# Optimization experiments

Hardware: AMD Instinct MI355X
Metric: run time of the kernel (lower is better)

Reference implementation:

```python
import jax, jax.numpy as jnp
import numpy as np

N = 1_000_000          # number of fusion candidate pairs
H, W = 200, 70400      # sparse buffer dims hard-coded in the module
FILL = -9999999.0


def _init_conv(k, co, ci):
    # torch Conv2d default init: U(-1/sqrt(fan_in), 1/sqrt(fan_in)), 1x1 kernel
    bound = 1.0 / np.sqrt(ci)
    kw, kb = jax.random.split(k)
    w = jax.random.uniform(kw, (co, ci), jnp.float32, -bound, bound)
    b = jax.random.uniform(kb, (co,), jnp.float32, -bound, bound)
    return w, b


def setup_inputs() -> dict:
    key = jax.random.key(0)
    ks = jax.random.split(key, 7)
    input_1 = jax.random.normal(ks[0], (1, 4, 1, N), dtype=jnp.float32)
    idx0 = jax.random.randint(ks[1], (N,), 0, H)   # row in [0,200)
    idx1 = jax.random.randint(ks[2], (N,), 0, W)   # col in [0,70400)
    tensor_index = jnp.stack([idx0, idx1], axis=1).astype(jnp.int64)
    w1, b1 = _init_conv(ks[3], 18, 4)
    w2, b2 = _init_conv(ks[4], 36, 18)
    w3, b3 = _init_conv(ks[5], 36, 36)
    w4, b4 = _init_conv(ks[6], 1, 36)
    return dict(input_1=input_1, tensor_index=tensor_index,
                w1=w1, b1=b1, w2=w2, b2=b2, w3=w3, b3=b3, w4=w4, b4=b4)


def _fuse_2d_3d(x, w1, b1, w2, b2, w3, b3, w4, b4):
    # x: (4, N); 1x1 convs over a (1,C,1,N) tensor == per-point channel matmuls
    h = jax.nn.relu(w1 @ x + b1[:, None])
    h = jax.nn.relu(w2 @ h + b2[:, None])
    h = jax.nn.relu(w3 @ h + b3[:, None])
    return w4 @ h + b4[:, None]  # (1, N)


def reference(input_1, tensor_index, w1, b1, w2, b2, w3, b3, w4, b4):
    base = jnp.full((1, H, W), FILL, dtype=input_1.dtype)

    def scatter_branch(_):
        feat = _fuse_2d_3d(input_1[0, :, 0, :], w1, b1, w2, b2, w3, b3, w4, b4)  # (1, N)
        out = base.at[:, tensor_index[:, 0], tensor_index[:, 1]].set(feat)
        return out, jnp.int32(1)

    def empty_branch(_):
        return base, jnp.int32(0)

    out_1, flag = jax.lax.cond(tensor_index[0, 0] == -1,
                               empty_branch, scatter_branch, None)
    # MaxPool2d([200,1]) over (C=1,H=200,W) -> max over H; squeeze+reshape -> (1, W, 1)
    x = jnp.max(out_1, axis=1)            # (1, W)
    return x.reshape(1, -1, 1), flag
```

## Files before the change

kernel.cpp:

```cpp
#include <hip/hip_runtime.h>

#define N_PTS 1000000
#define H_DIM 200
#define W_DIM 70400
#define FILL_V -9999999.0f

typedef float v2f __attribute__((ext_vector_type(2)));

__device__ __forceinline__ v2f fma2(v2f a, v2f b, v2f c) {
    return __builtin_elementwise_fma(a, b, c);
}

__global__ void __launch_bounds__(256) mlp_scatter_kernel(
    const float* __restrict__ input,
    const int* __restrict__ tindex,
    const float* __restrict__ w1, const float* __restrict__ b1,
    const float* __restrict__ w2, const float* __restrict__ b2,
    const float* __restrict__ w3, const float* __restrict__ b3,
    const float* __restrict__ w4, const float* __restrict__ b4,
    int* __restrict__ counts,
    uint2* __restrict__ list,
    int maxk)
{
    if (tindex[0] == -1) return;

    const int i = blockIdx.x * 256 + threadIdx.x;
    if (i >= N_PTS) return;

    const v2f* __restrict__ w1v = (const v2f*)w1;
    const v2f* __restrict__ w2v = (const v2f*)w2;
    const v2f* __restrict__ w3v = (const v2f*)w3;

    const v2f x01 = { input[0 * N_PTS + i], input[1 * N_PTS + i] };
    const v2f x23 = { input[2 * N_PTS + i], input[3 * N_PTS + i] };

    v2f h1v[9];
#pragma unroll
    for (int o = 0; o < 18; ++o) {
        v2f acc = { b1[o], 0.0f };
        acc = fma2(w1v[o * 2 + 0], x01, acc);
        acc = fma2(w1v[o * 2 + 1], x23, acc);
        const float h = fmaxf(acc.x + acc.y, 0.0f);
        if (o & 1) h1v[o >> 1].y = h; else h1v[o >> 1].x = h;
    }

    v2f h2v[18];
#pragma unroll
    for (int o = 0; o < 36; ++o) {
        v2f acc = { b2[o], 0.0f };
#pragma unroll
        for (int q = 0; q < 9; ++q)
            acc = fma2(w2v[o * 9 + q], h1v[q], acc);
        const float h = fmaxf(acc.x + acc.y, 0.0f);
        if (o & 1) h2v[o >> 1].y = h; else h2v[o >> 1].x = h;
    }

    float v = b4[0];
#pragma unroll
    for (int o = 0; o < 36; ++o) {
        v2f acc = { b3[o], 0.0f };
#pragma unroll
        for (int q = 0; q < 18; ++q)
            acc = fma2(w3v[o * 18 + q], h2v[q], acc);
        v = fmaf(w4[o], fmaxf(acc.x + acc.y, 0.0f), v);
    }

    const int2 hw = ((const int2*)tindex)[i];
    const int pos = atomicAdd(&counts[hw.y], 1);
    if (pos < maxk) {
        uint2 e;
        e.x = __float_as_uint(v);
        e.y = ((unsigned)i << 8) | (unsigned)hw.x;
        list[(size_t)hw.y * maxk + pos] = e;
    }
}

__global__ void __launch_bounds__(256) colmax_kernel(
    const int* __restrict__ tindex,
    const int* __restrict__ counts,
    const uint2* __restrict__ list,
    float* __restrict__ out,
    int maxk)
{
    __shared__ unsigned long long rowwin[4][200];
    const int lane = threadIdx.x;
    const int y    = threadIdx.y;
    const int w    = blockIdx.x * 4 + y;

    const bool empty = (tindex[0] == -1);

    if (blockIdx.x == 0 && lane == 0 && y == 0)
        out[W_DIM] = empty ? 0.0f : 1.0f;

    int c = 0;
    if (!empty) {
        c = counts[w];
        if (c > maxk) c = maxk;
    }

    unsigned long long* tbl = rowwin[y];
    tbl[lane]       = 0ull;
    tbl[lane + 64]  = 0ull;
    tbl[lane + 128] = 0ull;
    if (lane < 8) tbl[lane + 192] = 0ull;
    __syncthreads();

    uint2 e = make_uint2(0u, 0u);
    const bool have = (lane < c);
    if (have) {
        e = list[(size_t)w * maxk + lane];
        const unsigned long long key64 =
            ((unsigned long long)e.y << 32) | (unsigned long long)e.x;
        atomicMax(&tbl[e.y & 0xFFu], key64);
    }
    __syncthreads();

    float v = FILL_V;
    if (have) {
        const unsigned long long winner = tbl[e.y & 0xFFu];
        v = __uint_as_float((unsigned)(winner & 0xFFFFFFFFull));
    }
#pragma unroll
    for (int off = 32; off > 0; off >>= 1)
        v = fmaxf(v, __shfl_down(v, off, 64));

    if (lane == 0) out[w] = v;
}

extern "C" void kernel_launch(void* const* d_in, const int* in_sizes, int n_in,
                              void* d_out, int out_size, void* d_ws, size_t ws_size,
                              hipStream_t stream) {
    const float* input  = (const float*)d_in[0];
    const int*   tindex = (const int*)d_in[1];
    const float* w1 = (const float*)d_in[2];
    const float* b1 = (const float*)d_in[3];
    const float* w2 = (const float*)d_in[4];
    const float* b2 = (const float*)d_in[5];
    const float* w3 = (const float*)d_in[6];
    const float* b3 = (const float*)d_in[7];
    const float* w4 = (const float*)d_in[8];
    const float* b4 = (const float*)d_in[9];
    float* out = (float*)d_out;

    int*   counts = (int*)d_ws;
    uint2* list   = (uint2*)((char*)d_ws + (size_t)W_DIM * sizeof(int));

    size_t avail = (ws_size > (size_t)W_DIM * sizeof(int))
                       ? ws_size - (size_t)W_DIM * sizeof(int) : 0;
    int maxk = (int)(avail / ((size_t)W_DIM * sizeof(uint2)));
    if (maxk > 64) maxk = 64;
    if (maxk < 1)  maxk = 1;

    hipMemsetAsync(counts, 0, (size_t)W_DIM * sizeof(int), stream);

    mlp_scatter_kernel<<<(N_PTS + 255) / 256, 256, 0, stream>>>(
        input, tindex, w1, b1, w2, b2, w3, b3, w4, b4, counts, list, maxk);

    colmax_kernel<<<W_DIM / 4, dim3(64, 4), 0, stream>>>(
        tindex, counts, list, out, maxk);
}
```

Before: 173.6 us.

## Fuse memset, MLP scatter and column max into one cooperative persistent kernel

Replaces the memset plus two kernel launches with a single cooperative-groups kernel that zeroes counts, runs the MLP and scatter with a grid-stride loop, then does the per-column max, separated by grid-wide syncs. The aim is to remove launch and inter-kernel gaps. In exchange it adds grid.sync costs. The grid is capped at 2048 blocks, so occupancy may be lower than the original 3907-block launch, and the column phase now loops with block-wide barriers.

```diff
diff --git a/kernel.cpp b/kernel.cpp
--- a/kernel.cpp
+++ b/kernel.cpp
@@ -1,4 +1,7 @@
 #include <hip/hip_runtime.h>
+#include <hip/hip_cooperative_groups.h>
+
+namespace cg = cooperative_groups;
 
 #define N_PTS 1000000
 #define H_DIM 200
@@ -11,7 +14,7 @@
     return __builtin_elementwise_fma(a, b, c);
 }
 
-__global__ void __launch_bounds__(256) mlp_scatter_kernel(
+__global__ void __launch_bounds__(256) fused_kernel(
     const float* __restrict__ input,
     const int* __restrict__ tindex,
     const float* __restrict__ w1, const float* __restrict__ b1,
@@ -20,111 +23,116 @@
     const float* __restrict__ w4, const float* __restrict__ b4,
     int* __restrict__ counts,
     uint2* __restrict__ list,
-    int maxk)
+    int maxk,
+    float* __restrict__ out)
 {
-    if (tindex[0] == -1) return;
+    cg::grid_group grid = cg::this_grid();
+    const int tid      = blockIdx.x * 256 + threadIdx.x;
+    const int nthreads = gridDim.x * 256;
+    const bool empty   = (tindex[0] == -1);
 
-    const int i = blockIdx.x * 256 + threadIdx.x;
-    if (i >= N_PTS) return;
+    for (int k = tid; k < W_DIM; k += nthreads) counts[k] = 0;
+    grid.sync();
 
-    const v2f* __restrict__ w1v = (const v2f*)w1;
-    const v2f* __restrict__ w2v = (const v2f*)w2;
-    const v2f* __restrict__ w3v = (const v2f*)w3;
+    if (!empty) {
+        const v2f* __restrict__ w1v = (const v2f*)w1;
+        const v2f* __restrict__ w2v = (const v2f*)w2;
+        const v2f* __restrict__ w3v = (const v2f*)w3;
 
-    const v2f x01 = { input[0 * N_PTS + i], input[1 * N_PTS + i] };
-    const v2f x23 = { input[2 * N_PTS + i], input[3 * N_PTS + i] };
+        for (int i = tid; i < N_PTS; i += nthreads) {
+            const v2f x01 = { input[0 * N_PTS + i], input[1 * N_PTS + i] };
+            const v2f x23 = { input[2 * N_PTS + i], input[3 * N_PTS + i] };
 
-    v2f h1v[9];
+            v2f h1v[9];
 #pragma unroll
-    for (int o = 0; o < 18; ++o) {
-        v2f acc = { b1[o], 0.0f };
-        acc = fma2(w1v[o * 2 + 0], x01, acc);
-        acc = fma2(w1v[o * 2 + 1], x23, acc);
-        const float h = fmaxf(acc.x + acc.y, 0.0f);
-        if (o & 1) h1v[o >> 1].y = h; else h1v[o >> 1].x = h;
+            for (int o = 0; o < 18; ++o) {
+                v2f acc = { b1[o], 0.0f };
+                acc = fma2(w1v[o * 2 + 0], x01, acc);
+                acc = fma2(w1v[o * 2 + 1], x23, acc);
+                const float h = fmaxf(acc.x + acc.y, 0.0f);
+                if (o & 1) h1v[o >> 1].y = h; else h1v[o >> 1].x = h;
+            }
+
+            v2f h2v[18];
+#pragma unroll
+            for (int o = 0; o < 36; ++o) {
+                v2f acc = { b2[o], 0.0f };
+#pragma unroll
+                for (int q = 0; q < 9; ++q)
+                    acc = fma2(w2v[o * 9 + q], h1v[q], acc);
+                const float h = fmaxf(acc.x + acc.y, 0.0f);
+                if (o & 1) h2v[o >> 1].y = h; else h2v[o >> 1].x = h;
+            }
+
+            float v = b4[0];
+#pragma unroll
+            for (int o = 0; o < 36; ++o) {
+                v2f acc = { b3[o], 0.0f };
+#pragma unroll
+                for (int q = 0; q < 18; ++q)
+                    acc = fma2(w3v[o * 18 + q], h2v[q], acc);
+                v = fmaf(w4[o], fmaxf(acc.x + acc.y, 0.0f), v);
+            }
+
+            const int2 hw = ((const int2*)tindex)[i];
+            const int pos = atomicAdd(&counts[hw.y], 1);
+            if (pos < maxk) {
+                uint2 e;
+                e.x = __float_as_uint(v);
+                e.y = ((unsigned)i << 8) | (unsigned)hw.x;
+                list[(size_t)hw.y * maxk + pos] = e;
+            }
+        }
     }
+    __threadfence();
+    grid.sync();
 
-    v2f h2v[18];
+    __shared__ unsigned long long rowwin[4][200];
+    const int lane = threadIdx.x & 63;
+    const int wv   = threadIdx.x >> 6;
+    unsigned long long* tbl = rowwin[wv];
+    const int gw0    = blockIdx.x * 4 + wv;
+    const int nwaves = gridDim.x * 4;
+    const int iters  = (W_DIM + nwaves - 1) / nwaves;
+
+    if (tid == 0) out[W_DIM] = empty ? 0.0f : 1.0f;
+
+    for (int it = 0; it < iters; ++it) {
+        const int w = gw0 + it * nwaves;
+        const bool active = (w < W_DIM) && !empty;
+
+        tbl[lane]       = 0ull;
+        tbl[lane + 64]  = 0ull;
+        tbl[lane + 128] = 0ull;
+        if (lane < 8) tbl[lane + 192] = 0ull;
+        __syncthreads();
+
+        uint2 e = make_uint2(0u, 0u);
+        bool have = false;
+        if (active) {
+            int c = counts[w];
+            if (c > maxk) c = maxk;
+            have = (lane < c);
+            if (have) {
+                e = list[(size_t)w * maxk + lane];
+                const unsigned long long key64 =
+                    ((unsigned long long)e.y << 32) | (unsigned long long)e.x;
+                atomicMax(&tbl[e.y & 0xFFu], key64);
+            }
+        }
+        __syncthreads();
+
+        float v = FILL_V;
+        if (have) {
+            const unsigned long long winner = tbl[e.y & 0xFFu];
+            v = __uint_as_float((unsigned)(winner & 0xFFFFFFFFull));
+        }
 #pragma unroll
-    for (int o = 0; o < 36; ++o) {
-        v2f acc = { b2[o], 0.0f };
-#pragma unroll
-        for (int q = 0; q < 9; ++q)
-            acc = fma2(w2v[o * 9 + q], h1v[q], acc);
-        const float h = fmaxf(acc.x + acc.y, 0.0f);
-        if (o & 1) h2v[o >> 1].y = h; else h2v[o >> 1].x = h;
+        for (int off = 32; off > 0; off >>= 1)
+            v = fmaxf(v, __shfl_down(v, off, 64));
+
+        if (lane == 0 && w < W_DIM) out[w] = v;
     }
-
-    float v = b4[0];
-#pragma unroll
-    for (int o = 0; o < 36; ++o) {
-        v2f acc = { b3[o], 0.0f };
-#pragma unroll
-        for (int q = 0; q < 18; ++q)
-            acc = fma2(w3v[o * 18 + q], h2v[q], acc);
-        v = fmaf(w4[o], fmaxf(acc.x + acc.y, 0.0f), v);
-    }
-
-    const int2 hw = ((const int2*)tindex)[i];
-    const int pos = atomicAdd(&counts[hw.y], 1);
-    if (pos < maxk) {
-        uint2 e;
-        e.x = __float_as_uint(v);
-        e.y = ((unsigned)i << 8) | (unsigned)hw.x;
-        list[(size_t)hw.y * maxk + pos] = e;
-    }
-}
-
-__global__ void __launch_bounds__(256) colmax_kernel(
-    const int* __restrict__ tindex,
-    const int* __restrict__ counts,
-    const uint2* __restrict__ list,
-    float* __restrict__ out,
-    int maxk)
-{
-    __shared__ unsigned long long rowwin[4][200];
-    const int lane = threadIdx.x;
-    const int y    = threadIdx.y;
-    const int w    = blockIdx.x * 4 + y;
-
-    const bool empty = (tindex[0] == -1);
-
-    if (blockIdx.x == 0 && lane == 0 && y == 0)
-        out[W_DIM] = empty ? 0.0f : 1.0f;
-
-    int c = 0;
-    if (!empty) {
-        c = counts[w];
-        if (c > maxk) c = maxk;
-    }
-
-    unsigned long long* tbl = rowwin[y];
-    tbl[lane]       = 0ull;
-    tbl[lane + 64]  = 0ull;
-    tbl[lane + 128] = 0ull;
-    if (lane < 8) tbl[lane + 192] = 0ull;
-    __syncthreads();
-
-    uint2 e = make_uint2(0u, 0u);
-    const bool have = (lane < c);
-    if (have) {
-        e = list[(size_t)w * maxk + lane];
-        const unsigned long long key64 =
-            ((unsigned long long)e.y << 32) | (unsigned long long)e.x;
-        atomicMax(&tbl[e.y & 0xFFu], key64);
-    }
-    __syncthreads();
-
-    float v = FILL_V;
-    if (have) {
-        const unsigned long long winner = tbl[e.y & 0xFFu];
-        v = __uint_as_float((unsigned)(winner & 0xFFFFFFFFull));
-    }
-#pragma unroll
-    for (int off = 32; off > 0; off >>= 1)
-        v = fmaxf(v, __shfl_down(v, off, 64));
-
-    if (lane == 0) out[w] = v;
 }
 
 extern "C" void kernel_launch(void* const* d_in, const int* in_sizes, int n_in,
@@ -151,11 +159,17 @@
     if (maxk > 64) maxk = 64;
     if (maxk < 1)  maxk = 1;
 
-    hipMemsetAsync(counts, 0, (size_t)W_DIM * sizeof(int), stream);
+    int maxb = 0;
+    hipOccupancyMaxActiveBlocksPerMultiprocessor(&maxb, fused_kernel, 256, 0);
+    if (maxb < 1) maxb = 2;
+    int G = maxb * 256;
+    if (G > 2048) G = 2048;
 
-    mlp_scatter_kernel<<<(N_PTS + 255) / 256, 256, 0, stream>>>(
-        input, tindex, w1, b1, w2, b2, w3, b3, w4, b4, counts, list, maxk);
-
-    colmax_kernel<<<W_DIM / 4, dim3(64, 4), 0, stream>>>(
-        tindex, counts, list, out, maxk);
+    void* args[] = {
+        (void*)&input, (void*)&tindex,
+        (void*)&w1, (void*)&b1, (void*)&w2, (void*)&b2,
+        (void*)&w3, (void*)&b3, (void*)&w4, (void*)&b4,
+        (void*)&counts, (void*)&list, (void*)&maxk, (void*)&out
+    };
+    hipLaunchCooperativeKernel(fused_kernel, dim3(G), dim3(256), args, 0, stream);
 }
```

New measurement: 438.7 us. 2.53x slower.
